# Performance work log

Measured on AMD Instinct MI355X. Metric: run time of the kernel, lower is better.

The kernel has to match this reference:

```python
import jax, jax.numpy as jnp
import numpy as np
from jax import lax

DN = ('NCHW', 'OIHW', 'NCHW')


def conv2d(x, w, b, stride, pad):
    y = lax.conv_general_dilated(x, w, (stride, stride), [(pad, pad), (pad, pad)],
                                 dimension_numbers=DN)
    return y + b[None, :, None, None]


def conv2d_transpose(x, w, b):
    # k=4, s=2, p=1 transposed conv: lhs_dilation=2, padding k-1-p=2.
    # w is stored directly as OIHW for this dilated conv (reference params).
    y = lax.conv_general_dilated(x, w, (1, 1), [(2, 2), (2, 2)],
                                 lhs_dilation=(2, 2), dimension_numbers=DN)
    return y + b[None, :, None, None]


def setup_inputs() -> dict:
    key = jax.random.key(0)
    ks = jax.random.split(key, 16)
    D, K = 64, 512  # embedding_dim, num_embeddings
    C1, C2 = 128, 256

    def w(k, shape, fan_in):
        return (jax.random.normal(k, shape, jnp.float32) / np.sqrt(fan_in)).astype(jnp.float32)

    inp = {
        'x':   jax.random.normal(ks[0], (8, 3, 256, 256), jnp.float32),
        # encoder: two stride-2 conv stages (k=4,s=2,p=1) + ReLU
        'ew1': w(ks[1], (C1, 3, 4, 4), 3 * 16),   'eb1': jnp.zeros((C1,), jnp.float32),
        'ew2': w(ks[2], (C2, C1, 4, 4), C1 * 16), 'eb2': jnp.zeros((C2,), jnp.float32),
        # pre_vq 1x1 conv: C2 -> D
        'pvw': w(ks[3], (D, C2, 1, 1), C2),       'pvb': jnp.zeros((D,), jnp.float32),
        # codebook, uniform(-1/K, 1/K) as in the torch init
        'emb': jax.random.uniform(ks[4], (K, D), jnp.float32, -1.0 / K, 1.0 / K),
        # post_vq 3x3 conv: D -> C2
        'qvw': w(ks[5], (C2, D, 3, 3), D * 9),    'qvb': jnp.zeros((C2,), jnp.float32),
        # decoder: two stride-2 transposed conv stages
        'dw1': w(ks[6], (C1, C2, 4, 4), C2 * 16), 'db1': jnp.zeros((C1,), jnp.float32),
        'dw2': w(ks[7], (3, C1, 4, 4), C1 * 16),  'db2': jnp.zeros((3,), jnp.float32),
    }
    return inp


def vector_quantize(z_e, emb, commitment_cost):
    # z_e: [B, D, H, W] -> [B, H, W, D]
    inputs = jnp.transpose(z_e, (0, 2, 3, 1))
    B, H, W, D = inputs.shape
    K = emb.shape[0]
    flat = inputs.reshape(-1, D)                                   # [N, D]
    dist = (jnp.sum(flat * flat, axis=1, keepdims=True)
            + jnp.sum(emb * emb, axis=1)
            - 2.0 * jnp.matmul(flat, emb.T))                        # [N, K]
    idx = jnp.argmin(dist, axis=1)                                  # [N]
    encodings = jax.nn.one_hot(idx, K, dtype=flat.dtype)            # [N, K]
    quantized = emb[idx].reshape(B, H, W, D)                        # gather == encodings @ emb

    e_latent_loss = jnp.mean((lax.stop_gradient(quantized) - inputs) ** 2)
    q_latent_loss = jnp.mean((quantized - lax.stop_gradient(inputs)) ** 2)
    loss = q_latent_loss + commitment_cost * e_latent_loss

    quantized_st = inputs + lax.stop_gradient(quantized - inputs)   # straight-through
    avg_probs = jnp.mean(encodings, axis=0)
    perplexity = jnp.exp(-jnp.sum(avg_probs * jnp.log(avg_probs + 1e-10)))
    return loss, jnp.transpose(quantized_st, (0, 3, 1, 2)), perplexity, encodings


def reference(x, ew1, eb1, ew2, eb2, pvw, pvb, emb, qvw, qvb, dw1, db1, dw2, db2):
    commitment_cost = 0.25
    # encode
    h = jax.nn.relu(conv2d(x, ew1, eb1, 2, 1))    # [8,128,128,128]
    h = jax.nn.relu(conv2d(h, ew2, eb2, 2, 1))    # [8,256,64,64]
    z_e = conv2d(h, pvw, pvb, 1, 0)               # [8,64,64,64]
    # vector quantize
    loss, quantized, perplexity, _ = vector_quantize(z_e, emb, commitment_cost)
    # decode
    g = conv2d(quantized, qvw, qvb, 1, 1)         # [8,256,64,64]
    g = jax.nn.relu(conv2d_transpose(g, dw1, db1))  # [8,128,128,128]
    x_recon = conv2d_transpose(g, dw2, db2)       # [8,3,256,256]
    return (loss, x_recon, perplexity)
```

## Files before the change

kernel.cpp:

```cpp
#include <hip/hip_runtime.h>
#include <math.h>

typedef unsigned short u16;
typedef unsigned int uint;
typedef __attribute__((ext_vector_type(8))) short bh8;
typedef __attribute__((ext_vector_type(4))) float f32x4;

#define DEV __device__ __forceinline__

DEV u16 f2bf(float x) {
  uint u = __builtin_bit_cast(uint, x);
  return (u16)((u + 0x7FFFu + ((u >> 16) & 1u)) >> 16);
}
DEV float bf2f(u16 h) { return __builtin_bit_cast(float, (uint)h << 16); }

DEV int xcd_swz(int bid, int nb) {
  int c = nb >> 3;
  return (bid & 7) * c + (bid >> 3);
}

__global__ __launch_bounds__(256, 4) void conv1_f32(const float* __restrict__ src,
                                                    const float* __restrict__ Bt,
                                                    const float* __restrict__ bias,
                                                    uint* __restrict__ outu) {
  __shared__ __align__(16) float As[16*64];
  __shared__ __align__(16) float Bs[16*64];

  const int t = threadIdx.x;
  const int bid = (int)blockIdx.x;
  const int nt = bid & 1, m = bid >> 1;
  const int pl = t & 63, kb = t >> 6;
  const int p = m*64 + pl;
  const int n = p >> 14, h = (p >> 7) & 127, w = p & 127;
  const int ti = t & 15, tj = t >> 4;

  float acc[4][4];
  #pragma unroll
  for (int i = 0; i < 4; ++i)
    #pragma unroll
    for (int j = 0; j < 4; ++j) acc[i][j] = 0.f;

  for (int k0 = 0; k0 < 48; k0 += 16) {
    #pragma unroll
    for (int jj = 0; jj < 4; ++jj) {
      int kr = jj*4 + kb, k = k0 + kr;
      int ic = k >> 4, r = k & 15;
      int ih = 2*h - 1 + (r >> 2), iw = 2*w - 1 + (r & 3);
      As[kr*64 + pl] = ((unsigned)ih < 256u && (unsigned)iw < 256u)
        ? src[((n*3 + ic) << 16) + (ih << 8) + iw] : 0.f;
    }
    {
      int kr = t >> 4, c4 = t & 15;
      ((float4*)Bs)[kr*16 + c4] =
          *((const float4*)(Bt + (size_t)(k0 + kr)*128 + nt*64) + c4);
    }
    __syncthreads();
    #pragma unroll
    for (int kk = 0; kk < 16; ++kk) {
      float a[4], b[4];
      *(float4*)&a[0] = *(const float4*)&As[kk*64 + ti*4];
      *(float4*)&b[0] = *(const float4*)&Bs[kk*64 + tj*4];
      #pragma unroll
      for (int i = 0; i < 4; ++i)
        #pragma unroll
        for (int j = 0; j < 4; ++j)
          acc[i][j] += a[i]*b[j];
    }
    __syncthreads();
  }

  const int nn = m >> 8, hh = (m >> 1) & 127;
  const int woff2 = (m & 1) * 32;
  #pragma unroll
  for (int j = 0; j < 4; ++j) {
    const int oc = nt*64 + tj*4 + j;
    uint pk[4];
    #pragma unroll
    for (int q = 0; q < 4; ++q) {
      float v = fmaxf(acc[q][j] + bias[oc], 0.f);
      u16 hi = f2bf(v);
      u16 lo = f2bf(v - bf2f(hi));
      pk[q] = (uint)hi | ((uint)lo << 16);
    }
    uint* bp = outu + (size_t)(nn*128 + oc)*16384 + hh*128;
    *(uint2*)(bp + woff2 + ti*2)      = make_uint2(pk[0], pk[2]);
    *(uint2*)(bp + 64 + woff2 + ti*2) = make_uint2(pk[1], pk[3]);
  }
}

__global__ __launch_bounds__(256, 2) void conv2_mfma3(const uint* __restrict__ h1u,
                                                      const u16* __restrict__ Bh,
                                                      const u16* __restrict__ Bl,
                                                      const float* __restrict__ bias,
                                                      float* __restrict__ out) {
  __shared__ __align__(16) u16 Ah[128*40 + 32];
  __shared__ __align__(16) u16 Al[128*40 + 32];
  __shared__ __align__(16) u16 Bhs[128*40 + 32];
  __shared__ __align__(16) u16 Bls[128*40 + 32];

  const int t = threadIdx.x;
  const int bid = xcd_swz((int)blockIdx.x, (int)gridDim.x);
  const int nt = bid & 1, mt = bid >> 1;
  const int pl = t & 127, kb = t >> 7;
  const int p = mt*128 + pl;
  const int n = p >> 12, h = (p >> 6) & 63, w = p & 63;
  const int lane = t & 63, wv = t >> 6;
  const int lr = lane & 15, lg = lane >> 4;
  const int wm = wv & 1, wn = wv >> 1;

  int off[4]; uint mskd[4];
  off[0] = 64 + w - 1; mskd[0] = (w >= 1)  ? ~0u : 0u;
  off[1] = w;          mskd[1] = ~0u;
  off[2] = 64 + w;     mskd[2] = ~0u;
  off[3] = w + 1;      mskd[3] = (w <= 62) ? ~0u : 0u;

  f32x4 acc[4][4];
  #pragma unroll
  for (int fm = 0; fm < 4; ++fm)
    #pragma unroll
    for (int fn = 0; fn < 4; ++fn)
      #pragma unroll
      for (int q = 0; q < 4; ++q) acc[fm][fn][q] = 0.f;

  const int aw = pl*40 + kb*16;

  for (int k0 = 0; k0 < 2048; k0 += 32) {
    const int dy = k0 >> 9, icb = (k0 >> 2) & 127;
    const int ih = 2*h - 1 + dy;
    const uint mih = ((unsigned)ih < 128u) ? ~0u : 0u;
    const uint* pb = h1u + (size_t)(n*128 + icb + kb*4)*16384
                        + (((unsigned)ih < 128u) ? ih : 0)*128;
    uint m2[4];
    #pragma unroll
    for (int dx = 0; dx < 4; ++dx) m2[dx] = mskd[dx] & mih;

    uint raw[16];
    #pragma unroll
    for (int c = 0; c < 4; ++c)
      #pragma unroll
      for (int dx = 0; dx < 4; ++dx)
        raw[c*4 + dx] = pb[c*16384 + off[dx]] & m2[dx];

    uint hi8[8], lo8[8];
    #pragma unroll
    for (int q = 0; q < 8; ++q) {
      uint a = raw[2*q], b = raw[2*q+1];
      hi8[q] = (a & 0xffffu) | (b << 16);
      lo8[q] = (a >> 16) | (b & 0xffff0000u);
    }
    __syncthreads();
    *(uint4*)&Ah[aw]     = *(uint4*)&hi8[0];
    *(uint4*)&Ah[aw + 8] = *(uint4*)&hi8[4];
    *(uint4*)&Al[aw]     = *(uint4*)&lo8[0];
    *(uint4*)&Al[aw + 8] = *(uint4*)&lo8[4];
    #pragma unroll
    for (int i = 0; i < 2; ++i) {
      int id = i*256 + t, oc = id >> 2, ch = id & 3;
      size_t bo = (size_t)(nt*128 + oc)*2048 + k0 + ch*8;
      *(uint4*)&Bhs[oc*40 + ch*8] = *(const uint4*)(Bh + bo);
      *(uint4*)&Bls[oc*40 + ch*8] = *(const uint4*)(Bl + bo);
    }
    __syncthreads();

    bh8 afh[4], afl[4];
    #pragma unroll
    for (int fm = 0; fm < 4; ++fm) {
      const int r = (wm*64 + fm*16 + lr)*40 + lg*8;
      afh[fm] = *(const bh8*)&Ah[r];
      afl[fm] = *(const bh8*)&Al[r];
    }
    #pragma unroll
    for (int fn = 0; fn < 4; ++fn) {
      const int r = (wn*64 + fn*16 + lr)*40 + lg*8;
      bh8 bfh = *(const bh8*)&Bhs[r];
      bh8 bfl = *(const bh8*)&Bls[r];
      #pragma unroll
      for (int fm = 0; fm < 4; ++fm) {
        acc[fm][fn] = __builtin_amdgcn_mfma_f32_16x16x32_bf16(afh[fm], bfh, acc[fm][fn], 0,0,0);
        acc[fm][fn] = __builtin_amdgcn_mfma_f32_16x16x32_bf16(afl[fm], bfh, acc[fm][fn], 0,0,0);
        acc[fm][fn] = __builtin_amdgcn_mfma_f32_16x16x32_bf16(afh[fm], bfl, acc[fm][fn], 0,0,0);
      }
    }
  }

  #pragma unroll
  for (int fm = 0; fm < 4; ++fm) {
    const int pq = mt*128 + wm*64 + fm*16 + lg*4;
    const int nn = pq >> 12, hwq = pq & 4095;
    #pragma unroll
    for (int fn = 0; fn < 4; ++fn) {
      const int oc = nt*128 + wn*64 + fn*16 + lr;
      const float bv = bias[oc];
      float v0 = fmaxf(acc[fm][fn][0] + bv, 0.f);
      float v1 = fmaxf(acc[fm][fn][1] + bv, 0.f);
      float v2 = fmaxf(acc[fm][fn][2] + bv, 0.f);
      float v3 = fmaxf(acc[fm][fn][3] + bv, 0.f);
      *(float4*)(out + (((size_t)(nn*256 + oc)) << 12) + hwq) = make_float4(v0,v1,v2,v3);
    }
  }
}

__global__ __launch_bounds__(256, 3) void prevq_vq(const float* __restrict__ h2,
                                                   const float* __restrict__ btp,
                                                   const float* __restrict__ pvb,
                                                   const float* __restrict__ emb,
                                                   const float* __restrict__ Et,
                                                   const float* __restrict__ enrm,
                                                   uint* __restrict__ qz32,
                                                   int* __restrict__ hist,
                                                   float* __restrict__ loss_sum) {
  __shared__ __align__(16) float SM[10944 + 16];
  float* Zs   = SM;
  float* As   = SM + 4352;
  float* Bs   = SM + 4352 + 1024;
  float* Es   = SM + 4352;
  float* nrmS = SM + 4352 + 4224;
  float* redv = SM + 4352 + 4224 + 128;
  int*   redi = (int*)(redv + 1088);
  int*   sIdx = (int*)(redv + 2176);

  const int t = threadIdx.x;
  const int base = (int)blockIdx.x * 64;
  const int n = base >> 12, hwb = base & 4095;
  const int ti = t & 15, tj = t >> 4;

  {
    const int pl = t & 63, kb = t >> 6;
    const int hw = hwb + pl;
    float acc[4][4];
    #pragma unroll
    for (int i = 0; i < 4; ++i)
      #pragma unroll
      for (int j = 0; j < 4; ++j) acc[i][j] = 0.f;

    for (int k0 = 0; k0 < 256; k0 += 16) {
      #pragma unroll
      for (int jj = 0; jj < 4; ++jj) {
        int kr = jj*4 + kb;
        As[kr*64 + pl] = h2[((size_t)(n*256 + k0 + kr) << 12) + hw];
      }
      {
        int kr = t >> 4, c4 = t & 15;
        ((float4*)Bs)[kr*16 + c4] = *((const float4*)(btp + (size_t)(k0 + kr)*64) + c4);
      }
      __syncthreads();
      #pragma unroll
      for (int kk = 0; kk < 16; ++kk) {
        float a[4], b[4];
        *(float4*)&a[0] = *(const float4*)&As[kk*64 + ti*4];
        *(float4*)&b[0] = *(const float4*)&Bs[kk*64 + tj*4];
        #pragma unroll
        for (int i = 0; i < 4; ++i)
          #pragma unroll
          for (int j = 0; j < 4; ++j)
            acc[i][j] += a[i]*b[j];
      }
      __syncthreads();
    }
    #pragma unroll
    for (int j = 0; j < 4; ++j) {
      float bv = pvb[tj*4 + j];
      #pragma unroll
      for (int i = 0; i < 4; ++i)
        Zs[(tj*4 + j)*68 + ti*4 + i] = acc[i][j] + bv;
    }
  }

  float bv[4]; int bi[4];
  #pragma unroll
  for (int i = 0; i < 4; ++i) { bv[i] = 3.402823466e38f; bi[i] = 0; }

  for (int c = 0; c < 4; ++c) {
    float acc[4][8];
    #pragma unroll
    for (int i = 0; i < 4; ++i)
      #pragma unroll
      for (int j = 0; j < 8; ++j) acc[i][j] = 0.f;

    for (int hh = 0; hh < 2; ++hh) {
      __syncthreads();
      #pragma unroll
      for (int i = 0; i < 4; ++i) {
        int fid = i*256 + t, row = fid >> 5, c4 = fid & 31;
        *(float4*)&Es[row*132 + c4*4] =
            *(const float4*)(Et + (size_t)(hh*32 + row)*512 + c*128 + c4*4);
      }
      if (hh == 0 && t < 128) nrmS[t] = enrm[c*128 + t];
      __syncthreads();
      #pragma unroll 4
      for (int kk = 0; kk < 32; ++kk) {
        float4 a0 = *(const float4*)&Zs[(hh*32 + kk)*68 + ti*4];
        float4 b0 = *(const float4*)&Es[kk*132 + tj*8];
        float4 b1 = *(const float4*)&Es[kk*132 + tj*8 + 4];
        float a[4] = {a0.x, a0.y, a0.z, a0.w};
        float b[8] = {b0.x,b0.y,b0.z,b0.w, b1.x,b1.y,b1.z,b1.w};
        #pragma unroll
        for (int i = 0; i < 4; ++i)
          #pragma unroll
          for (int j = 0; j < 8; ++j)
            acc[i][j] += a[i]*b[j];
      }
    }
    #pragma unroll
    for (int j = 0; j < 8; ++j) {
      int code = c*128 + tj*8 + j;
      float nv = nrmS[tj*8 + j];
      #pragma unroll
      for (int i = 0; i < 4; ++i) {
        float d = nv - 2.f*acc[i][j];
        if (d < bv[i]) { bv[i] = d; bi[i] = code; }
      }
    }
  }

  __syncthreads();
  #pragma unroll
  for (int i = 0; i < 4; ++i) {
    redv[(ti*4 + i)*17 + tj] = bv[i];
    redi[(ti*4 + i)*17 + tj] = bi[i];
  }
  __syncthreads();
  if (t < 64) {
    float best = 3.402823466e38f; int bid = 0x7fffffff;
    #pragma unroll
    for (int j = 0; j < 16; ++j) {
      float v = redv[t*17 + j]; int ix = redi[t*17 + j];
      if (v < best || (v == best && ix < bid)) { best = v; bid = ix; }
    }
    sIdx[t] = bid;
  }
  __syncthreads();

  const int px = t & 63, grp = t >> 6;
  const int ix = sIdx[px];
  const float* er = emb + (size_t)ix * 64 + grp*16;
  uint* qb = qz32 + ((size_t)(n*32 + grp*8))*4096 + hwb + px;
  float ls = 0.f;
  #pragma unroll
  for (int dp = 0; dp < 8; ++dp) {
    float e0 = er[2*dp], e1 = er[2*dp + 1];
    float z0 = Zs[(grp*16 + 2*dp)*68 + px];
    float z1 = Zs[(grp*16 + 2*dp + 1)*68 + px];
    float d0 = e0 - z0, d1 = e1 - z1;
    ls += d0*d0 + d1*d1;
    qb[(size_t)dp * 4096] = (uint)f2bf(e0) | ((uint)f2bf(e1) << 16);
  }
  if (t < 64) atomicAdd(&hist[ix], 1);
  #pragma unroll
  for (int o = 32; o; o >>= 1) ls += __shfl_down(ls, o, 64);
  if ((t & 63) == 0) atomicAdd(loss_sum, ls);
}

__global__ void finalize_kernel(const int* __restrict__ hist,
                                const float* __restrict__ loss_sum,
                                float* __restrict__ out_loss,
                                float* __restrict__ out_perp) {
  __shared__ float red[512];
  int t = threadIdx.x;
  float pr = (float)hist[t] * (1.f/32768.f);
  red[t] = pr * logf(pr + 1e-10f);
  __syncthreads();
  for (int s = 256; s; s >>= 1) {
    if (t < s) red[t] += red[t + s];
    __syncthreads();
  }
  if (t == 0) {
    out_loss[0] = 1.25f * loss_sum[0] * (1.f/2097152.f);
    out_perp[0] = expf(-red[0]);
  }
}

enum { M_POSTVQ, M_DECONV1, M_DECONV2 };

template<int MODE> struct Cfg;
template<> struct Cfg<M_POSTVQ> { static constexpr int K=576,  BN=64, NOC=256, RELU=0, PAR=0; };
template<> struct Cfg<M_DECONV1>{ static constexpr int K=1024, BN=64, NOC=128, RELU=1, PAR=1; };
template<> struct Cfg<M_DECONV2>{ static constexpr int K=512,  BN=16, NOC=16,  RELU=0, PAR=1; };

template<int MODE>
__global__ __launch_bounds__(256, 4) void conv_mfma(const uint* __restrict__ srcu,
                                                    const u16* __restrict__ Bt,
                                                    const float* __restrict__ bias,
                                                    void* __restrict__ out_) {
  constexpr int K  = Cfg<MODE>::K;
  constexpr int BN = Cfg<MODE>::BN;
  constexpr int NT = Cfg<MODE>::NOC / BN;
  constexpr int FM = 2;
  constexpr int FN = BN / 16;

  __shared__ __align__(16) u16 As[128 * 72];
  __shared__ __align__(16) u16 Bs[BN * 72];

  const int t = threadIdx.x;
  int bid = xcd_swz((int)blockIdx.x, (int)gridDim.x);
  int par = 0;
  if constexpr (Cfg<MODE>::PAR) { par = bid & 3; bid >>= 2; }
  int nt = 0;
  if constexpr (NT > 1) { nt = bid % NT; bid /= NT; }
  const int mt = bid;
  const u16* Brow = Bt + ((size_t)par * Cfg<MODE>::NOC + (size_t)nt * BN) * K;

  const int pl = t & 127, kb = t >> 7;
  const int p = mt * 128 + pl;
  int n, h, w;
  if constexpr (MODE == M_DECONV2) { n = p >> 14; h = (p >> 7) & 127; w = p & 127; }
  else                             { n = p >> 12; h = (p >> 6) & 63;  w = p & 63;  }

  const int lane = t & 63, wv = t >> 6;
  const int lr = lane & 15, lg = lane >> 4;

  f32x4 acc[FM][FN];
  #pragma unroll
  for (int fm = 0; fm < FM; ++fm)
    #pragma unroll
    for (int fn = 0; fn < FN; ++fn)
      #pragma unroll
      for (int q = 0; q < 4; ++q) acc[fm][fn][q] = 0.f;

  for (int k0 = 0; k0 < K; k0 += 64) {
    const uint* up; bool ok;
    if constexpr (MODE == M_POSTVQ) {
      int r = k0 >> 6, kh = r / 3, kw = r - 3*kh;
      int ih = h - 1 + kh, iw = w - 1 + kw;
      ok = ((unsigned)ih < 64u) && ((unsigned)iw < 64u);
      up = srcu + ((size_t)(n*32 + kb*16)) * 4096
                + (ok ? ((ih << 6) + iw) : 0);
    } else if constexpr (MODE == M_DECONV1) {
      int j = k0 >> 8, icb = k0 & 255;
      int j1 = j >> 1, j0 = j & 1;
      int py = par >> 1, px = par & 1;
      int ih = h + py - 1 + j1, iw = w + px - 1 + j0;
      ok = ((unsigned)ih < 64u) && ((unsigned)iw < 64u);
      up = srcu + ((size_t)(n*128 + (icb >> 1) + kb*16)) * 4096
                + (ok ? ((ih << 6) + iw) : 0);
    } else {
      int tap = k0 >> 7, icb = k0 & 127;
      int j1 = tap >> 1, j0 = tap & 1;
      int qy = par >> 1, qx = par & 1;
      int ih = h - 1 + qy + j1, iw = w - 1 + qx + j0;
      ok = ((unsigned)ih < 128u) && ((unsigned)iw < 128u);
      int ipar = ((ih & 1) << 1) | (iw & 1);
      up = srcu + ((size_t)((n*4 + ipar)*64 + (icb >> 1) + kb*16)) * 4096
                + (ok ? (((ih >> 1) << 6) + (iw >> 1)) : 0);
    }
    uint raw[16];
    #pragma unroll
    for (int i = 0; i < 16; ++i)
      raw[i] = ok ? up[(size_t)i * 4096] : 0u;

    __syncthreads();
    #pragma unroll
    for (int i = 0; i < 4; ++i)
      *(uint4*)&As[pl*72 + kb*32 + i*8] =
          make_uint4(raw[4*i], raw[4*i+1], raw[4*i+2], raw[4*i+3]);

    constexpr int NBI = (BN*8 + 255) / 256;
    #pragma unroll
    for (int i = 0; i < NBI; ++i) {
      int id = i*256 + t;
      bool okb = true;
      if constexpr ((BN*8) % 256 != 0) okb = (id < BN*8);
      if (okb) {
        int oc = id >> 3, ch = id & 7;
        *(uint4*)&Bs[oc*72 + ch*8] = *(const uint4*)(Brow + (size_t)oc*K + k0 + ch*8);
      }
    }
    __syncthreads();

    #pragma unroll
    for (int ks = 0; ks < 2; ++ks) {
      bh8 af[FM];
      #pragma unroll
      for (int fm = 0; fm < FM; ++fm)
        af[fm] = *(const bh8*)&As[(wv*32 + fm*16 + lr)*72 + ks*32 + lg*8];
      #pragma unroll
      for (int fn = 0; fn < FN; ++fn) {
        bh8 bf = *(const bh8*)&Bs[(fn*16 + lr)*72 + ks*32 + lg*8];
        #pragma unroll
        for (int fm = 0; fm < FM; ++fm)
          acc[fm][fn] = __builtin_amdgcn_mfma_f32_16x16x32_bf16(af[fm], bf, acc[fm][fn], 0, 0, 0);
      }
    }
  }

  uint*  outu32 = (uint*)out_;
  float* outf   = (float*)out_;
  const bool evn = !(lr & 1);
  #pragma unroll
  for (int fm = 0; fm < FM; ++fm) {
    const int pq = mt*128 + wv*32 + fm*16 + lg*4;
    #pragma unroll
    for (int fn = 0; fn < FN; ++fn) {
      const int oc = nt*BN + fn*16 + lr;
      float bvv;
      if constexpr (MODE == M_DECONV2) bvv = (lr < 3) ? bias[oc] : 0.f;
      else                             bvv = bias[oc];
      float v[4];
      #pragma unroll
      for (int q = 0; q < 4; ++q) {
        v[q] = acc[fm][fn][q] + bvv;
        if constexpr (Cfg<MODE>::RELU) v[q] = fmaxf(v[q], 0.f);
      }
      if constexpr (MODE == M_DECONV2) {
        if (lr < 3) {
          const int nn = pq >> 14;
          const int hq = (pq >> 7) & 127, wq = pq & 127;
          const int qy = par >> 1, qx = par & 1;
          const int oh = 2*hq + qy;
          float* ob = outf + (((size_t)(nn*3 + oc)) << 16) + (oh << 8) + qx;
          ob[2*wq]     = v[0];
          ob[2*wq + 2] = v[1];
          ob[2*wq + 4] = v[2];
          ob[2*wq + 6] = v[3];
        }
      } else {
        float pv[4];
        #pragma unroll
        for (int q = 0; q < 4; ++q) pv[q] = __shfl_xor(v[q], 1, 64);
        uint pk[4];
        #pragma unroll
        for (int q = 0; q < 4; ++q) {
          u16 a = f2bf(evn ? v[q] : pv[q]);
          u16 b = f2bf(evn ? pv[q] : v[q]);
          pk[q] = (uint)a | ((uint)b << 16);
        }
        const int nn = pq >> 12, hwq = pq & 4095;
        size_t pbase;
        if constexpr (MODE == M_POSTVQ)
          pbase = ((size_t)(nn*128 + (oc >> 1))) * 4096 + hwq;
        else
          pbase = ((size_t)((nn*4 + par)*64 + (oc >> 1))) * 4096 + hwq;
        if (evn) *(uint2*)(outu32 + pbase)     = make_uint2(pk[0], pk[1]);
        else     *(uint2*)(outu32 + pbase + 2) = make_uint2(pk[2], pk[3]);
      }
    }
  }
}

__global__ void prep_enc(const float* __restrict__ ew1, const float* __restrict__ ew2,
                         const float* __restrict__ pvw, const float* __restrict__ emb,
                         float* bt1, u16* bt2h, u16* bt2l, float* btp,
                         float* Et, float* enrm) {
  int i = blockIdx.x * 256 + threadIdx.x;
  if (i < 6144) {
    int k = i >> 7, oc = i & 127;
    bt1[i] = ew1[oc*48 + k];
  } else if ((i -= 6144) < 524288) {
    int oc = i >> 11, k = i & 2047;
    int dy = k >> 9, ic = (k >> 2) & 127, dx = k & 3;
    float v = ew2[oc*2048 + ic*16 + dy*4 + dx];
    u16 hi = f2bf(v);
    bt2h[i] = hi;
    bt2l[i] = f2bf(v - bf2f(hi));
  } else if ((i -= 524288) < 16384) {
    int k = i >> 6, oc = i & 63;
    btp[i] = pvw[oc*256 + k];
  } else if ((i -= 16384) < 32768) {
    int d = i >> 9, code = i & 511;
    Et[i] = emb[code*64 + d];
  } else if ((i -= 32768) < 512) {
    float s = 0.f;
    const float* er = emb + (size_t)i * 64;
    #pragma unroll
    for (int d = 0; d < 64; ++d) s += er[d]*er[d];
    enrm[i] = s;
  }
}

__global__ void prep_dec(const float* __restrict__ qvw, const float* __restrict__ dw1,
                         const float* __restrict__ dw2,
                         u16* btq, u16* btd, u16* btd2) {
  int i = blockIdx.x * 256 + threadIdx.x;
  if (i < 147456) {
    int oc = i / 576, rem = i - oc*576, r = rem >> 6, ic = rem & 63;
    btq[i] = f2bf(qvw[oc*576 + ic*9 + r]);
  } else if ((i -= 147456) < 524288) {
    int pr = i >> 17, oc = (i >> 10) & 127, j = (i >> 8) & 3, ic = i & 255;
    int py = pr >> 1, px = pr & 1, j1 = j >> 1, j0 = j & 1;
    btd[i] = f2bf(dw1[oc*4096 + ic*16 + (py + 2*j1)*4 + (px + 2*j0)]);
  } else if ((i -= 524288) < 32768) {
    int q = i >> 13, oc = (i >> 9) & 15, tap = (i >> 7) & 3, ic = i & 127;
    int qy = q >> 1, qx = q & 1, j1 = tap >> 1, j0 = tap & 1;
    btd2[i] = (oc < 3) ? f2bf(dw2[oc*2048 + ic*16 + (qy + 2*j1)*4 + (qx + 2*j0)]) : (u16)0;
  }
}

extern "C" void kernel_launch(void* const* d_in, const int* in_sizes, int n_in,
                              void* d_out, int out_size, void* d_ws, size_t ws_size,
                              hipStream_t stream) {
  (void)in_sizes; (void)n_in; (void)ws_size;
  const float* x   = (const float*)d_in[0];
  const float* ew1 = (const float*)d_in[1];
  const float* eb1 = (const float*)d_in[2];
  const float* ew2 = (const float*)d_in[3];
  const float* eb2 = (const float*)d_in[4];
  const float* pvw = (const float*)d_in[5];
  const float* pvb = (const float*)d_in[6];
  const float* emb = (const float*)d_in[7];
  const float* qvw = (const float*)d_in[8];
  const float* qvb = (const float*)d_in[9];
  const float* dw1 = (const float*)d_in[10];
  const float* db1 = (const float*)d_in[11];
  const float* dw2 = (const float*)d_in[12];
  const float* db2 = (const float*)d_in[13];
  float* out = (float*)d_out;

  char* ws = (char*)d_ws;
  uint*  h1u  = (uint*) (ws);
  float* h2   = (float*)(ws + 67108864);
  uint*  qz32 = (uint*) (ws + 109051904);
  int*   hist = (int*)  (ws + 113246208);
  float* lsum = (float*)(ws + 113248256);
  float* bt1  = (float*)(ws + 113248320);
  float* btp  = (float*)(ws + 113272896);
  u16*   bt2h = (u16*)  (ws + 113338432);
  u16*   bt2l = (u16*)  (ws + 114387008);
  u16*   btq  = (u16*)  (ws + 115435584);
  u16*   btd  = (u16*)  (ws + 115730496);
  u16*   btd2 = (u16*)  (ws + 116779072);
  float* Et   = (float*)(ws + 116844608);
  float* enrm = (float*)(ws + 116975680);
  uint* g32  = (uint*)(ws + 67108864);
  uint* g232 = (uint*)ws;

  hipMemsetAsync(hist, 0, 2048 + 64, stream);
  prep_enc<<<2266, 256, 0, stream>>>(ew1, ew2, pvw, emb, bt1, bt2h, bt2l, btp, Et, enrm);
  prep_dec<<<2752, 256, 0, stream>>>(qvw, dw1, dw2, btq, btd, btd2);

  conv1_f32<<<4096, 256, 0, stream>>>(x, bt1, eb1, h1u);
  conv2_mfma3<<<512, 256, 0, stream>>>(h1u, bt2h, bt2l, eb2, h2);

  prevq_vq<<<512, 256, 0, stream>>>(h2, btp, pvb, emb, Et, enrm, qz32, hist, lsum);
  finalize_kernel<<<1, 512, 0, stream>>>(hist, lsum, out, out + (out_size - 1));

  conv_mfma<M_POSTVQ> <<<1024, 256, 0, stream>>>(qz32, btq, qvb, g32);
  conv_mfma<M_DECONV1><<<2048, 256, 0, stream>>>(g32, btd, db1, g232);
  conv_mfma<M_DECONV2><<<4096, 256, 0, stream>>>(g232, btd2, db2, out + 1);
}
```

Measured before the change: 398.6 us.

## Enlarge conv tiles to 128x128 with 64-deep K steps in encoder and decoder GEMMs

conv2_mfma3 now stages 64 K-elements per iteration instead of 32, halving the number of barrier pairs and loop iterations. The post-VQ and deconv1 convolutions move to a new 128x128 output tile kernel with a 2x2 wave layout, which halves the grid and doubles the reuse of each staged A and B fragment. Deconv2 gets its own specialised kernel. The larger tiles raise LDS and register use per block, which can reduce occupancy.

```diff
diff --git a/kernel.cpp b/kernel.cpp
--- a/kernel.cpp
+++ b/kernel.cpp
@@ -93,10 +93,10 @@
                                                       const u16* __restrict__ Bl,
                                                       const float* __restrict__ bias,
                                                       float* __restrict__ out) {
-  __shared__ __align__(16) u16 Ah[128*40 + 32];
-  __shared__ __align__(16) u16 Al[128*40 + 32];
-  __shared__ __align__(16) u16 Bhs[128*40 + 32];
-  __shared__ __align__(16) u16 Bls[128*40 + 32];
+  __shared__ __align__(16) u16 Ah[128*72 + 32];
+  __shared__ __align__(16) u16 Al[128*72 + 32];
+  __shared__ __align__(16) u16 Bhs[128*72 + 32];
+  __shared__ __align__(16) u16 Bls[128*72 + 32];
 
   const int t = threadIdx.x;
   const int bid = xcd_swz((int)blockIdx.x, (int)gridDim.x);
@@ -122,63 +122,67 @@
       #pragma unroll
       for (int q = 0; q < 4; ++q) acc[fm][fn][q] = 0.f;
 
-  const int aw = pl*40 + kb*16;
-
-  for (int k0 = 0; k0 < 2048; k0 += 32) {
+  const int aw = pl*72 + kb*32;
+
+  for (int k0 = 0; k0 < 2048; k0 += 64) {
     const int dy = k0 >> 9, icb = (k0 >> 2) & 127;
     const int ih = 2*h - 1 + dy;
     const uint mih = ((unsigned)ih < 128u) ? ~0u : 0u;
-    const uint* pb = h1u + (size_t)(n*128 + icb + kb*4)*16384
+    const uint* pb = h1u + (size_t)(n*128 + icb + kb*8)*16384
                         + (((unsigned)ih < 128u) ? ih : 0)*128;
     uint m2[4];
     #pragma unroll
     for (int dx = 0; dx < 4; ++dx) m2[dx] = mskd[dx] & mih;
 
-    uint raw[16];
-    #pragma unroll
-    for (int c = 0; c < 4; ++c)
+    uint raw[32];
+    #pragma unroll
+    for (int c = 0; c < 8; ++c)
       #pragma unroll
       for (int dx = 0; dx < 4; ++dx)
         raw[c*4 + dx] = pb[c*16384 + off[dx]] & m2[dx];
 
-    uint hi8[8], lo8[8];
-    #pragma unroll
-    for (int q = 0; q < 8; ++q) {
+    uint hi16[16], lo16[16];
+    #pragma unroll
+    for (int q = 0; q < 16; ++q) {
       uint a = raw[2*q], b = raw[2*q+1];
-      hi8[q] = (a & 0xffffu) | (b << 16);
-      lo8[q] = (a >> 16) | (b & 0xffff0000u);
-    }
-    __syncthreads();
-    *(uint4*)&Ah[aw]     = *(uint4*)&hi8[0];
-    *(uint4*)&Ah[aw + 8] = *(uint4*)&hi8[4];
-    *(uint4*)&Al[aw]     = *(uint4*)&lo8[0];
-    *(uint4*)&Al[aw + 8] = *(uint4*)&lo8[4];
-    #pragma unroll
-    for (int i = 0; i < 2; ++i) {
-      int id = i*256 + t, oc = id >> 2, ch = id & 3;
+      hi16[q] = (a & 0xffffu) | (b << 16);
+      lo16[q] = (a >> 16) | (b & 0xffff0000u);
+    }
+    __syncthreads();
+    #pragma unroll
+    for (int i = 0; i < 4; ++i) {
+      *(uint4*)&Ah[aw + i*8] = *(uint4*)&hi16[4*i];
+      *(uint4*)&Al[aw + i*8] = *(uint4*)&lo16[4*i];
+    }
+    #pragma unroll
+    for (int i = 0; i < 4; ++i) {
+      int id = i*256 + t, oc = id >> 3, ch = id & 7;
       size_t bo = (size_t)(nt*128 + oc)*2048 + k0 + ch*8;
-      *(uint4*)&Bhs[oc*40 + ch*8] = *(const uint4*)(Bh + bo);
-      *(uint4*)&Bls[oc*40 + ch*8] = *(const uint4*)(Bl + bo);
-    }
-    __syncthreads();
-
-    bh8 afh[4], afl[4];
-    #pragma unroll
-    for (int fm = 0; fm < 4; ++fm) {
-      const int r = (wm*64 + fm*16 + lr)*40 + lg*8;
-      afh[fm] = *(const bh8*)&Ah[r];
-      afl[fm] = *(const bh8*)&Al[r];
-    }
-    #pragma unroll
-    for (int fn = 0; fn < 4; ++fn) {
-      const int r = (wn*64 + fn*16 + lr)*40 + lg*8;
-      bh8 bfh = *(const bh8*)&Bhs[r];
-      bh8 bfl = *(const bh8*)&Bls[r];
+      *(uint4*)&Bhs[oc*72 + ch*8] = *(const uint4*)(Bh + bo);
+      *(uint4*)&Bls[oc*72 + ch*8] = *(const uint4*)(Bl + bo);
+    }
+    __syncthreads();
+
+    #pragma unroll
+    for (int ks = 0; ks < 2; ++ks) {
+      bh8 afh[4], afl[4];
       #pragma unroll
       for (int fm = 0; fm < 4; ++fm) {
-        acc[fm][fn] = __builtin_amdgcn_mfma_f32_16x16x32_bf16(afh[fm], bfh, acc[fm][fn], 0,0,0);
-        acc[fm][fn] = __builtin_amdgcn_mfma_f32_16x16x32_bf16(afl[fm], bfh, acc[fm][fn], 0,0,0);
-        acc[fm][fn] = __builtin_amdgcn_mfma_f32_16x16x32_bf16(afh[fm], bfl, acc[fm][fn], 0,0,0);
+        const int r = (wm*64 + fm*16 + lr)*72 + ks*32 + lg*8;
+        afh[fm] = *(const bh8*)&Ah[r];
+        afl[fm] = *(const bh8*)&Al[r];
+      }
+      #pragma unroll
+      for (int fn = 0; fn < 4; ++fn) {
+        const int r = (wn*64 + fn*16 + lr)*72 + ks*32 + lg*8;
+        bh8 bfh = *(const bh8*)&Bhs[r];
+        bh8 bfl = *(const bh8*)&Bls[r];
+        #pragma unroll
+        for (int fm = 0; fm < 4; ++fm) {
+          acc[fm][fn] = __builtin_amdgcn_mfma_f32_16x16x32_bf16(afh[fm], bfh, acc[fm][fn], 0,0,0);
+          acc[fm][fn] = __builtin_amdgcn_mfma_f32_16x16x32_bf16(afl[fm], bfh, acc[fm][fn], 0,0,0);
+          acc[fm][fn] = __builtin_amdgcn_mfma_f32_16x16x32_bf16(afh[fm], bfl, acc[fm][fn], 0,0,0);
+        }
       }
     }
   }
@@ -372,50 +376,38 @@
 
 enum { M_POSTVQ, M_DECONV1, M_DECONV2 };
 
-template<int MODE> struct Cfg;
-template<> struct Cfg<M_POSTVQ> { static constexpr int K=576,  BN=64, NOC=256, RELU=0, PAR=0; };
-template<> struct Cfg<M_DECONV1>{ static constexpr int K=1024, BN=64, NOC=128, RELU=1, PAR=1; };
-template<> struct Cfg<M_DECONV2>{ static constexpr int K=512,  BN=16, NOC=16,  RELU=0, PAR=1; };
-
 template<int MODE>
-__global__ __launch_bounds__(256, 4) void conv_mfma(const uint* __restrict__ srcu,
-                                                    const u16* __restrict__ Bt,
-                                                    const float* __restrict__ bias,
-                                                    void* __restrict__ out_) {
-  constexpr int K  = Cfg<MODE>::K;
-  constexpr int BN = Cfg<MODE>::BN;
-  constexpr int NT = Cfg<MODE>::NOC / BN;
-  constexpr int FM = 2;
-  constexpr int FN = BN / 16;
-
-  __shared__ __align__(16) u16 As[128 * 72];
-  __shared__ __align__(16) u16 Bs[BN * 72];
+__global__ __launch_bounds__(256, 4) void dec_mfma128(const uint* __restrict__ srcu,
+                                                      const u16* __restrict__ Bt,
+                                                      const float* __restrict__ bias,
+                                                      uint* __restrict__ out32) {
+  constexpr int K = (MODE == M_POSTVQ) ? 576 : 1024;
+  __shared__ __align__(16) u16 As[128*72 + 32];
+  __shared__ __align__(16) u16 Bs[128*72 + 32];
 
   const int t = threadIdx.x;
   int bid = xcd_swz((int)blockIdx.x, (int)gridDim.x);
-  int par = 0;
-  if constexpr (Cfg<MODE>::PAR) { par = bid & 3; bid >>= 2; }
-  int nt = 0;
-  if constexpr (NT > 1) { nt = bid % NT; bid /= NT; }
-  const int mt = bid;
-  const u16* Brow = Bt + ((size_t)par * Cfg<MODE>::NOC + (size_t)nt * BN) * K;
+  int par = 0, nt = 0, mt;
+  if constexpr (MODE == M_DECONV1) { par = bid & 3; mt = bid >> 2; }
+  else                             { nt = bid & 1;  mt = bid >> 1; }
+  const u16* Brow = Bt + (size_t)((MODE == M_DECONV1) ? par*128 : nt*128) * K;
 
   const int pl = t & 127, kb = t >> 7;
-  const int p = mt * 128 + pl;
-  int n, h, w;
-  if constexpr (MODE == M_DECONV2) { n = p >> 14; h = (p >> 7) & 127; w = p & 127; }
-  else                             { n = p >> 12; h = (p >> 6) & 63;  w = p & 63;  }
-
+  const int p = mt*128 + pl;
+  const int n = p >> 12, h = (p >> 6) & 63, w = p & 63;
   const int lane = t & 63, wv = t >> 6;
   const int lr = lane & 15, lg = lane >> 4;
-
-  f32x4 acc[FM][FN];
-  #pragma unroll
-  for (int fm = 0; fm < FM; ++fm)
-    #pragma unroll
-    for (int fn = 0; fn < FN; ++fn)
+  const int wm = wv & 1, wn = wv >> 1;
+
+  f32x4 acc[4][4];
+  #pragma unroll
+  for (int fm = 0; fm < 4; ++fm)
+    #pragma unroll
+    for (int fn = 0; fn < 4; ++fn)
       #pragma unroll
       for (int q = 0; q < 4; ++q) acc[fm][fn][q] = 0.f;
+
+  const int aw = pl*72 + kb*32;
 
   for (int k0 = 0; k0 < K; k0 += 64) {
     const uint* up; bool ok;
@@ -425,7 +417,7 @@
       ok = ((unsigned)ih < 64u) && ((unsigned)iw < 64u);
       up = srcu + ((size_t)(n*32 + kb*16)) * 4096
                 + (ok ? ((ih << 6) + iw) : 0);
-    } else if constexpr (MODE == M_DECONV1) {
+    } else {
       int j = k0 >> 8, icb = k0 & 255;
       int j1 = j >> 1, j0 = j & 1;
       int py = par >> 1, px = par & 1;
@@ -433,16 +425,113 @@
       ok = ((unsigned)ih < 64u) && ((unsigned)iw < 64u);
       up = srcu + ((size_t)(n*128 + (icb >> 1) + kb*16)) * 4096
                 + (ok ? ((ih << 6) + iw) : 0);
-    } else {
-      int tap = k0 >> 7, icb = k0 & 127;
-      int j1 = tap >> 1, j0 = tap & 1;
-      int qy = par >> 1, qx = par & 1;
-      int ih = h - 1 + qy + j1, iw = w - 1 + qx + j0;
-      ok = ((unsigned)ih < 128u) && ((unsigned)iw < 128u);
-      int ipar = ((ih & 1) << 1) | (iw & 1);
-      up = srcu + ((size_t)((n*4 + ipar)*64 + (icb >> 1) + kb*16)) * 4096
-                + (ok ? (((ih >> 1) << 6) + (iw >> 1)) : 0);
-    }
+    }
+    uint raw[16];
+    #pragma unroll
+    for (int i = 0; i < 16; ++i)
+      raw[i] = ok ? up[(size_t)i * 4096] : 0u;
+
+    __syncthreads();
+    #pragma unroll
+    for (int i = 0; i < 4; ++i)
+      *(uint4*)&As[aw + i*8] =
+          make_uint4(raw[4*i], raw[4*i+1], raw[4*i+2], raw[4*i+3]);
+
+    #pragma unroll
+    for (int i = 0; i < 4; ++i) {
+      int id = i*256 + t, oc = id >> 3, ch = id & 7;
+      *(uint4*)&Bs[oc*72 + ch*8] = *(const uint4*)(Brow + (size_t)oc*K + k0 + ch*8);
+    }
+    __syncthreads();
+
+    #pragma unroll
+    for (int ks = 0; ks < 2; ++ks) {
+      bh8 af[4];
+      #pragma unroll
+      for (int fm = 0; fm < 4; ++fm)
+        af[fm] = *(const bh8*)&As[(wm*64 + fm*16 + lr)*72 + ks*32 + lg*8];
+      #pragma unroll
+      for (int fn = 0; fn < 4; ++fn) {
+        bh8 bf = *(const bh8*)&Bs[(wn*64 + fn*16 + lr)*72 + ks*32 + lg*8];
+        #pragma unroll
+        for (int fm = 0; fm < 4; ++fm)
+          acc[fm][fn] = __builtin_amdgcn_mfma_f32_16x16x32_bf16(af[fm], bf, acc[fm][fn], 0, 0, 0);
+      }
+    }
+  }
+
+  const bool evn = !(lr & 1);
+  #pragma unroll
+  for (int fm = 0; fm < 4; ++fm) {
+    const int pq = mt*128 + wm*64 + fm*16 + lg*4;
+    const int nn = pq >> 12, hwq = pq & 4095;
+    #pragma unroll
+    for (int fn = 0; fn < 4; ++fn) {
+      const int oc = nt*128 + wn*64 + fn*16 + lr;
+      const float bvv = bias[oc];
+      float v[4];
+      #pragma unroll
+      for (int q = 0; q < 4; ++q) {
+        v[q] = acc[fm][fn][q] + bvv;
+        if constexpr (MODE == M_DECONV1) v[q] = fmaxf(v[q], 0.f);
+      }
+      float pv[4];
+      #pragma unroll
+      for (int q = 0; q < 4; ++q) pv[q] = __shfl_xor(v[q], 1, 64);
+      uint pk[4];
+      #pragma unroll
+      for (int q = 0; q < 4; ++q) {
+        u16 a = f2bf(evn ? v[q] : pv[q]);
+        u16 b = f2bf(evn ? pv[q] : v[q]);
+        pk[q] = (uint)a | ((uint)b << 16);
+      }
+      size_t pbase;
+      if constexpr (MODE == M_POSTVQ)
+        pbase = ((size_t)(nn*128 + (oc >> 1))) * 4096 + hwq;
+      else
+        pbase = ((size_t)((nn*4 + par)*64 + (oc >> 1))) * 4096 + hwq;
+      if (evn) *(uint2*)(out32 + pbase)     = make_uint2(pk[0], pk[1]);
+      else     *(uint2*)(out32 + pbase + 2) = make_uint2(pk[2], pk[3]);
+    }
+  }
+}
+
+__global__ __launch_bounds__(256, 4) void deconv2_mfma(const uint* __restrict__ srcu,
+                                                       const u16* __restrict__ Bt,
+                                                       const float* __restrict__ bias,
+                                                       float* __restrict__ outf) {
+  constexpr int K = 512, BN = 16;
+  __shared__ __align__(16) u16 As[128 * 72];
+  __shared__ __align__(16) u16 Bs[BN * 72];
+
+  const int t = threadIdx.x;
+  int bid = xcd_swz((int)blockIdx.x, (int)gridDim.x);
+  int par = bid & 3; bid >>= 2;
+  const int mt = bid;
+  const u16* Brow = Bt + (size_t)par * BN * K;
+
+  const int pl = t & 127, kb = t >> 7;
+  const int p = mt * 128 + pl;
+  const int n = p >> 14, h = (p >> 7) & 127, w = p & 127;
+
+  const int lane = t & 63, wv = t >> 6;
+  const int lr = lane & 15, lg = lane >> 4;
+
+  f32x4 acc[2];
+  #pragma unroll
+  for (int fm = 0; fm < 2; ++fm)
+    #pragma unroll
+    for (int q = 0; q < 4; ++q) acc[fm][q] = 0.f;
+
+  for (int k0 = 0; k0 < K; k0 += 64) {
+    int tap = k0 >> 7, icb = k0 & 127;
+    int j1 = tap >> 1, j0 = tap & 1;
+    int qy = par >> 1, qx = par & 1;
+    int ih = h - 1 + qy + j1, iw = w - 1 + qx + j0;
+    bool ok = ((unsigned)ih < 128u) && ((unsigned)iw < 128u);
+    int ipar = ((ih & 1) << 1) | (iw & 1);
+    const uint* up = srcu + ((size_t)((n*4 + ipar)*64 + (icb >> 1) + kb*16)) * 4096
+                          + (ok ? (((ih >> 1) << 6) + (iw >> 1)) : 0);
     uint raw[16];
     #pragma unroll
     for (int i = 0; i < 16; ++i)
@@ -453,14 +542,9 @@
     for (int i = 0; i < 4; ++i)
       *(uint4*)&As[pl*72 + kb*32 + i*8] =
           make_uint4(raw[4*i], raw[4*i+1], raw[4*i+2], raw[4*i+3]);
-
-    constexpr int NBI = (BN*8 + 255) / 256;
-    #pragma unroll
-    for (int i = 0; i < NBI; ++i) {
-      int id = i*256 + t;
-      bool okb = true;
-      if constexpr ((BN*8) % 256 != 0) okb = (id < BN*8);
-      if (okb) {
+    {
+      int id = t;
+      if (id < BN*8) {
         int oc = id >> 3, ch = id & 7;
         *(uint4*)&Bs[oc*72 + ch*8] = *(const uint4*)(Brow + (size_t)oc*K + k0 + ch*8);
       }
@@ -469,70 +553,32 @@
 
     #pragma unroll
     for (int ks = 0; ks < 2; ++ks) {
-      bh8 af[FM];
-      #pragma unroll
-      for (int fm = 0; fm < FM; ++fm)
+      bh8 af[2];
+      #pragma unroll
+      for (int fm = 0; fm < 2; ++fm)
         af[fm] = *(const bh8*)&As[(wv*32 + fm*16 + lr)*72 + ks*32 + lg*8];
-      #pragma unroll
-      for (int fn = 0; fn < FN; ++fn) {
-        bh8 bf = *(const bh8*)&Bs[(fn*16 + lr)*72 + ks*32 + lg*8];
-        #pragma unroll
-        for (int fm = 0; fm < FM; ++fm)
-          acc[fm][fn] = __builtin_amdgcn_mfma_f32_16x16x32_bf16(af[fm], bf, acc[fm][fn], 0, 0, 0);
-      }
-    }
-  }
-
-  uint*  outu32 = (uint*)out_;
-  float* outf   = (float*)out_;
-  const bool evn = !(lr & 1);
-  #pragma unroll
-  for (int fm = 0; fm < FM; ++fm) {
+      bh8 bf = *(const bh8*)&Bs[lr*72 + ks*32 + lg*8];
+      #pragma unroll
+      for (int fm = 0; fm < 2; ++fm)
+        acc[fm] = __builtin_amdgcn_mfma_f32_16x16x32_bf16(af[fm], bf, acc[fm], 0, 0, 0);
+    }
+  }
+
+  #pragma unroll
+  for (int fm = 0; fm < 2; ++fm) {
     const int pq = mt*128 + wv*32 + fm*16 + lg*4;
-    #pragma unroll
-    for (int fn = 0; fn < FN; ++fn) {
-      const int oc = nt*BN + fn*16 + lr;
-      float bvv;
-      if constexpr (MODE == M_DECONV2) bvv = (lr < 3) ? bias[oc] : 0.f;
-      else                             bvv = bias[oc];
-      float v[4];
-      #pragma unroll
-      for (int q = 0; q < 4; ++q) {
-        v[q] = acc[fm][fn][q] + bvv;
-        if constexpr (Cfg<MODE>::RELU) v[q] = fmaxf(v[q], 0.f);
-      }
-      if constexpr (MODE == M_DECONV2) {
-        if (lr < 3) {
-          const int nn = pq >> 14;
-          const int hq = (pq >> 7) & 127, wq = pq & 127;
-          const int qy = par >> 1, qx = par & 1;
-          const int oh = 2*hq + qy;
-          float* ob = outf + (((size_t)(nn*3 + oc)) << 16) + (oh << 8) + qx;
-          ob[2*wq]     = v[0];
-          ob[2*wq + 2] = v[1];
-          ob[2*wq + 4] = v[2];
-          ob[2*wq + 6] = v[3];
-        }
-      } else {
-        float pv[4];
-        #pragma unroll
-        for (int q = 0; q < 4; ++q) pv[q] = __shfl_xor(v[q], 1, 64);
-        uint pk[4];
-        #pragma unroll
-        for (int q = 0; q < 4; ++q) {
-          u16 a = f2bf(evn ? v[q] : pv[q]);
-          u16 b = f2bf(evn ? pv[q] : v[q]);
-          pk[q] = (uint)a | ((uint)b << 16);
-        }
-        const int nn = pq >> 12, hwq = pq & 4095;
-        size_t pbase;
-        if constexpr (MODE == M_POSTVQ)
-          pbase = ((size_t)(nn*128 + (oc >> 1))) * 4096 + hwq;
-        else
-          pbase = ((size_t)((nn*4 + par)*64 + (oc >> 1))) * 4096 + hwq;
-        if (evn) *(uint2*)(outu32 + pbase)     = make_uint2(pk[0], pk[1]);
-        else     *(uint2*)(outu32 + pbase + 2) = make_uint2(pk[2], pk[3]);
-      }
+    const int oc = lr;
+    if (oc < 3) {
+      const float bvv = bias[oc];
+      const int nn = pq >> 14;
+      const int hq = (pq >> 7) & 127, wq = pq & 127;
+      const int qy = par >> 1, qx = par & 1;
+      const int oh = 2*hq + qy;
+      float* ob = outf + (((size_t)(nn*3 + oc)) << 16) + (oh << 8) + qx;
+      ob[2*wq]     = acc[fm][0] + bvv;
+      ob[2*wq + 2] = acc[fm][1] + bvv;
+      ob[2*wq + 4] = acc[fm][2] + bvv;
+      ob[2*wq + 6] = acc[fm][3] + bvv;
     }
   }
 }
@@ -633,7 +679,7 @@
   prevq_vq<<<512, 256, 0, stream>>>(h2, btp, pvb, emb, Et, enrm, qz32, hist, lsum);
   finalize_kernel<<<1, 512, 0, stream>>>(hist, lsum, out, out + (out_size - 1));
 
-  conv_mfma<M_POSTVQ> <<<1024, 256, 0, stream>>>(qz32, btq, qvb, g32);
-  conv_mfma<M_DECONV1><<<2048, 256, 0, stream>>>(g32, btd, db1, g232);
-  conv_mfma<M_DECONV2><<<4096, 256, 0, stream>>>(g232, btd2, db2, out + 1);
-}
+  dec_mfma128<M_POSTVQ> <<<512,  256, 0, stream>>>(qz32, btq, qvb, g32);
+  dec_mfma128<M_DECONV1><<<1024, 256, 0, stream>>>(g32, btd, db1, g232);
+  deconv2_mfma<<<4096, 256, 0, stream>>>(g232, btd2, db2, out + 1);
+}
```

Result: no change. 399.5 us (+0.2%).
